# Optimization experiments

Measured on AMD Instinct MI355X. Metric: run time of the kernel, lower is better.

## Reference

```python
import jax, jax.numpy as jnp
import numpy as np

B, T, D = 2, 4096, 768
H = 12
HD = D // H  # 64
SCALE = 1.0 / np.sqrt(HD)


def setup_inputs() -> dict:
    key = jax.random.key(0)
    k1, k2, k3 = jax.random.split(key, 3)
    x = jax.random.normal(k1, (B, T, D), dtype=jnp.float32)
    W_qkv = jax.random.normal(k2, (D, 3 * D), dtype=jnp.float32) * (1.0 / np.sqrt(D))
    b_qkv = jnp.zeros((3 * D,), dtype=jnp.float32)
    W_out = jax.random.normal(k3, (D, D), dtype=jnp.float32) * (1.0 / np.sqrt(D))
    b_out = jnp.zeros((D,), dtype=jnp.float32)
    return {"x": x, "W_qkv": W_qkv, "b_qkv": b_qkv, "W_out": W_out, "b_out": b_out}


def reference(x, W_qkv, b_qkv, W_out, b_out):
    Bx, Tx, C = x.shape
    qkv = x @ W_qkv + b_qkv                                  # [B,T,3D]
    qkv = qkv.reshape(Bx, Tx, 3, H, HD).transpose(2, 0, 3, 1, 4)  # [3,B,H,T,hd]
    q, k, v = qkv[0], qkv[1], qkv[2]
    scores = jnp.einsum('bhqd,bhkd->bhqk', q, k) * SCALE      # [B,H,T,T]
    causal = jnp.tril(jnp.ones((Tx, Tx), dtype=bool))
    scores = jnp.where(causal[None, None], scores, -jnp.inf)
    attn = jax.nn.softmax(scores, axis=-1)
    out = jnp.einsum('bhqk,bhkd->bhqd', attn, v)              # [B,H,T,hd]
    out = out.transpose(0, 2, 1, 3).reshape(Bx, Tx, C)        # [B,T,D]
    return out @ W_out + b_out
```

## Files before the change

### kernel.cpp

```cpp
#include <hip/hip_runtime.h>
#include <cstdint>
#include <cstddef>

typedef _Float16 f16x8 __attribute__((ext_vector_type(8)));
typedef _Float16 f16x4 __attribute__((ext_vector_type(4)));
typedef float    f32x4 __attribute__((ext_vector_type(4)));

#define AS_GLOBAL __attribute__((address_space(1)))
#define AS_LDS    __attribute__((address_space(3)))

__device__ __forceinline__ void load16_to_lds(const _Float16* g, _Float16* l) {
    __builtin_amdgcn_global_load_lds((const AS_GLOBAL void*)g, (AS_LDS void*)l, 16, 0, 0);
}

#define BB   2
#define TT   4096
#define DD   768
#define NH   12
#define HDIM 64
#define D3   2304
#define SC2  (0.125f * 1.44269504088896f)

__global__ __launch_bounds__(256) void prep(const float* __restrict__ x,
                                            _Float16* __restrict__ Xh,
                                            const float* __restrict__ Wqkv,
                                            _Float16* __restrict__ Wqkvt,
                                            const float* __restrict__ Wout,
                                            _Float16* __restrict__ Wot) {
    const int bid = blockIdx.x, tid = threadIdx.x;
    if (bid < 6144) {
        const int i = bid * 1024 + tid * 4;
        float4 v = *(const float4*)(x + i);
        f16x4 h;
        h[0] = (_Float16)v.x; h[1] = (_Float16)v.y;
        h[2] = (_Float16)v.z; h[3] = (_Float16)v.w;
        *(f16x4*)(Xh + i) = h;
        return;
    }
    __shared__ float tile[32][33];
    const float* in; _Float16* out; int C, bx, by;
    if (bid < 7872) {
        const int t = bid - 6144;
        in = Wqkv; out = Wqkvt; C = 2304;
        bx = (t % 72) * 32; by = (t / 72) * 32;
    } else {
        const int t = bid - 7872;
        in = Wout; out = Wot; C = 768;
        bx = (t % 24) * 32; by = (t / 24) * 32;
    }
    const int R = 768;
    const int tx = tid & 31, ty = tid >> 5;
#pragma unroll
    for (int j = 0; j < 32; j += 8)
        tile[ty + j][tx] = in[(size_t)(by + ty + j) * C + bx + tx];
    __syncthreads();
#pragma unroll
    for (int j = 0; j < 32; j += 8)
        out[(size_t)(bx + ty + j) * R + by + tx] = (_Float16)tile[tx][ty + j];
}

template <typename OutT>
__device__ __forceinline__ void gemm_body(const _Float16* __restrict__ A,
                                          const _Float16* __restrict__ Bt,
                                          const float* __restrict__ bias, bool bias_row,
                                          OutT* __restrict__ C, int N, int K,
                                          int m0, int n0,
                                          _Float16* As, _Float16* Bs) {
    const int tid  = threadIdx.x;
    const int wave = tid >> 6, lane = tid & 63, quad = lane >> 4, l16 = lane & 15;
    const int wm = (wave & 1) * 64, wn = (wave >> 1) * 64;
    const int rowc = lane >> 3, part = lane & 7;

    f32x4 acc[4][4];
#pragma unroll
    for (int i = 0; i < 4; ++i)
#pragma unroll
        for (int n = 0; n < 4; ++n) acc[i][n] = f32x4{0.f, 0.f, 0.f, 0.f};

    for (int k0 = 0; k0 < K; k0 += 64) {
        __syncthreads();
#pragma unroll
        for (int cc = 0; cc < 4; ++cc) {
            const int ch = wave * 4 + cc;
            load16_to_lds(A  + (size_t)(m0 + ch * 8 + rowc) * K + k0 + part * 8,
                          As + ch * 512);
            load16_to_lds(Bt + (size_t)(n0 + ch * 8 + rowc) * K + k0 + part * 8,
                          Bs + ch * 512);
        }
        __syncthreads();
#pragma unroll
        for (int i = 0; i < 4; ++i) {
            f16x8 a0 = *(const f16x8*)(As + (wm + i * 16 + l16) * 64 + quad * 8);
            f16x8 a1 = *(const f16x8*)(As + (wm + i * 16 + l16) * 64 + 32 + quad * 8);
#pragma unroll
            for (int n = 0; n < 4; ++n) {
                f16x8 b0 = *(const f16x8*)(Bs + (wn + n * 16 + l16) * 64 + quad * 8);
                f16x8 b1 = *(const f16x8*)(Bs + (wn + n * 16 + l16) * 64 + 32 + quad * 8);
                acc[i][n] = __builtin_amdgcn_mfma_f32_16x16x32_f16(a0, b0, acc[i][n], 0, 0, 0);
                acc[i][n] = __builtin_amdgcn_mfma_f32_16x16x32_f16(a1, b1, acc[i][n], 0, 0, 0);
            }
        }
    }
#pragma unroll
    for (int i = 0; i < 4; ++i)
#pragma unroll
        for (int n = 0; n < 4; ++n)
#pragma unroll
            for (int r = 0; r < 4; ++r) {
                const int row = m0 + wm + i * 16 + quad * 4 + r;
                const int col = n0 + wn + n * 16 + l16;
                const float bv = bias_row ? bias[row] : bias[col];
                C[(size_t)row * N + col] = (OutT)(acc[i][n][r] + bv);
            }
}

__global__ __launch_bounds__(256) void gemm_qkv(const _Float16* __restrict__ Xh,
                                                const _Float16* __restrict__ Wqkvt,
                                                const float* __restrict__ bqkv,
                                                _Float16* __restrict__ QKh,
                                                _Float16* __restrict__ VtG) {
    __shared__ __align__(16) _Float16 As[128 * 64];
    __shared__ __align__(16) _Float16 Bs[128 * 64];
    const int bid = blockIdx.x;
    if (bid < 768) {
        const int bx = bid % 12, by = bid / 12;
        gemm_body<_Float16>(Xh, Wqkvt, bqkv, false, QKh, 1536, DD,
                            by * 128, bx * 128, As, Bs);
    } else {
        const int t = bid - 768;
        const int bx = t % 64, by = t / 64;
        gemm_body<_Float16>(Wqkvt + (size_t)1536 * DD, Xh, bqkv + 1536, true, VtG,
                            8192, DD, by * 128, bx * 128, As, Bs);
    }
}

__global__ __launch_bounds__(256) void gemm_out(const _Float16* __restrict__ A,
                                                const _Float16* __restrict__ Bt,
                                                const float* __restrict__ bias,
                                                float* __restrict__ C) {
    __shared__ __align__(16) _Float16 As[128 * 64];
    __shared__ __align__(16) _Float16 Bs[128 * 64];
    gemm_body<float>(A, Bt, bias, false, C, DD, DD,
                     (int)blockIdx.y * 128, (int)blockIdx.x * 128, As, Bs);
}

__global__ __launch_bounds__(256) void attn_kernel(const _Float16* __restrict__ qk,
                                                   const _Float16* __restrict__ vt,
                                                   _Float16* __restrict__ ao) {
    __shared__ __align__(16) _Float16 Ks[2][64 * 64];
    __shared__ __align__(16) _Float16 Vs[2][64 * 64];
    __shared__ __align__(16) _Float16 Ps[4][16 * 64];

    const int L    = blockIdx.x;
    const int xcd  = L & 7;
    const int r_   = L >> 3;
    const int gIdx = r_ >> 5;
    const int x    = r_ & 31;
    const int g    = gIdx * 8 + xcd;
    const int b = g / NH, h = g % NH;

    const int tid = threadIdx.x;
    const int wave = tid >> 6, lane = tid & 63, quad = lane >> 4, l16 = lane & 15;

    f16x8 ones;
#pragma unroll
    for (int j = 0; j < 8; ++j) ones[j] = (_Float16)1.0f;

    int vK[2], vV[2];
#pragma unroll
    for (int p = 0; p < 2; ++p) {
        const int j  = wave * 16 + p * 8 + (lane >> 3);
        const int sig = (j & 15) * 4 + (j >> 4);
        const int cdk = (lane & 7) ^ (j & 7);
        vK[p] = (b * TT + sig) * 1536 + DD + h * HDIM + cdk * 8;
        vV[p] = (h * HDIM + j) * 8192 + b * TT + cdk * 8;
    }
    auto stage = [&](int buf, int k0) {
        const int kK = k0 * 1536;
#pragma unroll
        for (int p = 0; p < 2; ++p) {
            load16_to_lds(qk + (vK[p] + kK), Ks[buf] + (wave * 16 + p * 8) * 64);
            load16_to_lds(vt + (vV[p] + k0), Vs[buf] + (wave * 16 + p * 8) * 64);
        }
    };

    _Float16* pw[4];
#pragma unroll
    for (int r = 0; r < 4; ++r) {
        const int row = quad * 4 + r;
        pw[r] = Ps[wave] + row * 64 + (((l16 >> 1) ^ (row & 7)) * 8) + (l16 & 1) * 4;
    }
    const _Float16* pr[2];
#pragma unroll
    for (int kh = 0; kh < 2; ++kh)
        pr[kh] = Ps[wave] + l16 * 64 + (((kh * 4 + quad) ^ (l16 & 7)) * 8);

    auto process = [&](int qt) {
        const int q0 = qt * 64;
        const int nkt = qt + 1;
        const int qrow = q0 + wave * 16 + quad * 4;
        f16x8 aq[2];
        {
            const int qoff = (b * TT + q0 + wave * 16 + l16) * 1536 + h * HDIM + quad * 8;
            const _Float16 sc = (_Float16)SC2;
            aq[0] = *(const f16x8*)(qk + qoff) * sc;
            aq[1] = *(const f16x8*)(qk + qoff + 32) * sc;
        }
        f32x4 o[4], lac;
#pragma unroll
        for (int n = 0; n < 4; ++n) o[n] = f32x4{0.f, 0.f, 0.f, 0.f};
        lac = f32x4{0.f, 0.f, 0.f, 0.f};

        __syncthreads();
        stage(0, 0);
        int cur = 0;
        for (int kt = 0; kt < nkt; ++kt) {
            __syncthreads();
            if (kt + 1 < nkt) stage(cur ^ 1, (kt + 1) * 64);

            f32x4 s[4];
#pragma unroll
            for (int n = 0; n < 4; ++n) s[n] = f32x4{0.f, 0.f, 0.f, 0.f};
#pragma unroll
            for (int kh = 0; kh < 2; ++kh)
#pragma unroll
                for (int n = 0; n < 4; ++n) {
                    const int pos = (kh * 4 + quad) ^ (l16 & 7);
                    f16x8 bk = *(const f16x8*)(Ks[cur] + (n * 16 + l16) * 64 + pos * 8);
                    s[n] = __builtin_amdgcn_mfma_f32_16x16x32_f16(aq[kh], bk, s[n], 0, 0, 0);
                }

            if (kt == nkt - 1) {
#pragma unroll
                for (int n = 0; n < 4; ++n) {
                    const int kg = kt * 64 + l16 * 4 + n;
#pragma unroll
                    for (int r = 0; r < 4; ++r)
                        if (kg > qrow + r) s[n][r] = -1e30f;
                }
            }

#pragma unroll
            for (int r = 0; r < 4; ++r) {
                f16x4 pk;
#pragma unroll
                for (int n = 0; n < 4; ++n)
                    pk[n] = (_Float16)__builtin_amdgcn_exp2f(s[n][r]);
                *(f16x4*)pw[r] = pk;
            }

#pragma unroll
            for (int kh = 0; kh < 2; ++kh) {
                f16x8 ap = *(const f16x8*)pr[kh];
                lac = __builtin_amdgcn_mfma_f32_16x16x32_f16(ap, ones, lac, 0, 0, 0);
#pragma unroll
                for (int n = 0; n < 4; ++n) {
                    const int posv = (kh * 4 + quad) ^ (l16 & 7);
                    f16x8 bv = *(const f16x8*)(Vs[cur] + (n * 16 + l16) * 64 + posv * 8);
                    o[n] = __builtin_amdgcn_mfma_f32_16x16x32_f16(ap, bv, o[n], 0, 0, 0);
                }
            }
            cur ^= 1;
        }

#pragma unroll
        for (int r = 0; r < 4; ++r) {
            const float inv = 1.0f / lac[r];
            const int ooff = (b * TT + qrow + r) * DD + h * HDIM + l16;
#pragma unroll
            for (int n = 0; n < 4; ++n)
                ao[ooff + n * 16] = (_Float16)(o[n][r] * inv);
        }
    };

    process(63 - x);
    process(x);
}

extern "C" void kernel_launch(void* const* d_in, const int* in_sizes, int n_in,
                              void* d_out, int out_size, void* d_ws, size_t ws_size,
                              hipStream_t stream) {
    const float* x     = (const float*)d_in[0];
    const float* Wqkv  = (const float*)d_in[1];
    const float* bqkv  = (const float*)d_in[2];
    const float* Wout  = (const float*)d_in[3];
    const float* bout  = (const float*)d_in[4];
    float* out = (float*)d_out;

    char* ws = (char*)d_ws;
    _Float16* Xh    = (_Float16*)ws;  ws += (size_t)BB * TT * DD * 2;
    _Float16* Wqkvt = (_Float16*)ws;  ws += (size_t)D3 * DD * 2;
    _Float16* Wot   = (_Float16*)ws;  ws += (size_t)DD * DD * 2;
    _Float16* QKh   = (_Float16*)ws;  ws += (size_t)BB * TT * 1536 * 2;
    _Float16* VtG   = (_Float16*)ws;  ws += (size_t)DD * BB * TT * 2;
    _Float16* AOh   = (_Float16*)ws;  ws += (size_t)BB * TT * DD * 2;

    prep<<<8448, 256, 0, stream>>>(x, Xh, Wqkv, Wqkvt, Wout, Wot);

    gemm_qkv<<<1152, 256, 0, stream>>>(Xh, Wqkvt, bqkv, QKh, VtG);

    attn_kernel<<<768, 256, 0, stream>>>(QKh, VtG, AOh);

    gemm_out<<<dim3(DD / 128, (BB * TT) / 128), 256, 0, stream>>>(AOh, Wot, bout, out);
}
```

Baseline: 257.6 us.

## Software-pipeline attention: overlap next tile's QK with previous tile's PV

```diff
diff --git a/kernel.cpp b/kernel.cpp
--- a/kernel.cpp
+++ b/kernel.cpp
@@ -149,7 +149,7 @@
                                                    _Float16* __restrict__ ao) {
     __shared__ __align__(16) _Float16 Ks[2][64 * 64];
     __shared__ __align__(16) _Float16 Vs[2][64 * 64];
-    __shared__ __align__(16) _Float16 Ps[4][16 * 64];
+    __shared__ __align__(16) _Float16 Ps[2][4][16 * 64];
 
     const int L    = blockIdx.x;
     const int xcd  = L & 7;
@@ -175,25 +175,29 @@
         vK[p] = (b * TT + sig) * 1536 + DD + h * HDIM + cdk * 8;
         vV[p] = (h * HDIM + j) * 8192 + b * TT + cdk * 8;
     }
-    auto stage = [&](int buf, int k0) {
+    auto stageK = [&](int buf, int k0) {
         const int kK = k0 * 1536;
 #pragma unroll
-        for (int p = 0; p < 2; ++p) {
+        for (int p = 0; p < 2; ++p)
             load16_to_lds(qk + (vK[p] + kK), Ks[buf] + (wave * 16 + p * 8) * 64);
+    };
+    auto stageV = [&](int buf, int k0) {
+#pragma unroll
+        for (int p = 0; p < 2; ++p)
             load16_to_lds(vt + (vV[p] + k0), Vs[buf] + (wave * 16 + p * 8) * 64);
-        }
     };
 
-    _Float16* pw[4];
+    _Float16* const PsW = &Ps[0][wave][0];
+    int pwo[4];
 #pragma unroll
     for (int r = 0; r < 4; ++r) {
         const int row = quad * 4 + r;
-        pw[r] = Ps[wave] + row * 64 + (((l16 >> 1) ^ (row & 7)) * 8) + (l16 & 1) * 4;
-    }
-    const _Float16* pr[2];
+        pwo[r] = row * 64 + (((l16 >> 1) ^ (row & 7)) * 8) + (l16 & 1) * 4;
+    }
+    int pro[2];
 #pragma unroll
     for (int kh = 0; kh < 2; ++kh)
-        pr[kh] = Ps[wave] + l16 * 64 + (((kh * 4 + quad) ^ (l16 & 7)) * 8);
+        pro[kh] = l16 * 64 + (((kh * 4 + quad) ^ (l16 & 7)) * 8);
 
     auto process = [&](int qt) {
         const int q0 = qt * 64;
@@ -211,13 +215,29 @@
         for (int n = 0; n < 4; ++n) o[n] = f32x4{0.f, 0.f, 0.f, 0.f};
         lac = f32x4{0.f, 0.f, 0.f, 0.f};
 
+        auto pv = [&](int pbuf, int vbuf) {
+#pragma unroll
+            for (int kh = 0; kh < 2; ++kh) {
+                f16x8 ap = *(const f16x8*)(PsW + pbuf * 4096 + pro[kh]);
+                lac = __builtin_amdgcn_mfma_f32_16x16x32_f16(ap, ones, lac, 0, 0, 0);
+#pragma unroll
+                for (int n = 0; n < 4; ++n) {
+                    const int posv = (kh * 4 + quad) ^ (l16 & 7);
+                    f16x8 bv = *(const f16x8*)(Vs[vbuf] + (n * 16 + l16) * 64 + posv * 8);
+                    o[n] = __builtin_amdgcn_mfma_f32_16x16x32_f16(ap, bv, o[n], 0, 0, 0);
+                }
+            }
+        };
+
         __syncthreads();
-        stage(0, 0);
+        stageK(0, 0);
         int cur = 0;
         for (int kt = 0; kt < nkt; ++kt) {
             __syncthreads();
-            if (kt + 1 < nkt) stage(cur ^ 1, (kt + 1) * 64);
-
+            if (kt + 1 < nkt) stageK(cur ^ 1, (kt + 1) * 64);
+            stageV(cur, kt * 64);
+
+            __builtin_amdgcn_s_setprio(1);
             f32x4 s[4];
 #pragma unroll
             for (int n = 0; n < 4; ++n) s[n] = f32x4{0.f, 0.f, 0.f, 0.f};
@@ -230,6 +250,9 @@
                     s[n] = __builtin_amdgcn_mfma_f32_16x16x32_f16(aq[kh], bk, s[n], 0, 0, 0);
                 }
 
+            if (kt > 0) pv(cur ^ 1, cur ^ 1);
+            __builtin_amdgcn_s_setprio(0);
+
             if (kt == nkt - 1) {
 #pragma unroll
                 for (int n = 0; n < 4; ++n) {
@@ -246,22 +269,13 @@
 #pragma unroll
                 for (int n = 0; n < 4; ++n)
                     pk[n] = (_Float16)__builtin_amdgcn_exp2f(s[n][r]);
-                *(f16x4*)pw[r] = pk;
-            }
-
-#pragma unroll
-            for (int kh = 0; kh < 2; ++kh) {
-                f16x8 ap = *(const f16x8*)pr[kh];
-                lac = __builtin_amdgcn_mfma_f32_16x16x32_f16(ap, ones, lac, 0, 0, 0);
-#pragma unroll
-                for (int n = 0; n < 4; ++n) {
-                    const int posv = (kh * 4 + quad) ^ (l16 & 7);
-                    f16x8 bv = *(const f16x8*)(Vs[cur] + (n * 16 + l16) * 64 + posv * 8);
-                    o[n] = __builtin_amdgcn_mfma_f32_16x16x32_f16(ap, bv, o[n], 0, 0, 0);
-                }
+                *(f16x4*)(PsW + cur * 4096 + pwo[r]) = pk;
             }
             cur ^= 1;
         }
+
+        __syncthreads();
+        pv(cur ^ 1, cur ^ 1);
 
 #pragma unroll
         for (int r = 0; r < 4; ++r) {
```

After: 248.0 us. 3.7% less time.
